# Performance work log

Hardware: AMD Instinct MI355X
Metric: run time of the kernel (lower is better)

## Reference

```python
import jax, jax.numpy as jnp
import numpy as np

B, L, D, H, V, NBARS = 128, 256, 256, 256, 130, 17


def _lstm(x, h, c, Wih, Whh, bih, bhh):
    # torch nn.LSTMCell math
    g = x @ Wih.T + h @ Whh.T + (bih + bhh)
    i, f, gg, o = jnp.split(g, 4, axis=-1)
    c2 = jax.nn.sigmoid(f) * c + jax.nn.sigmoid(i) * jnp.tanh(gg)
    return jax.nn.sigmoid(o) * jnp.tanh(c2), c2


def setup_inputs() -> dict:
    key = jax.random.key(0)
    ks = jax.random.split(key, 10)
    s = 0.05
    return dict(
        c=jax.random.normal(ks[0], (B, NBARS, D), jnp.float32),
        target=jax.random.randint(ks[1], (3, B, L), 0, V),
        length=L,
        W_hid=jax.random.normal(ks[2], (2 * D, D), jnp.float32) * s,
        b_hid=jnp.zeros((2 * D,), jnp.float32),
        W1_ih=jax.random.normal(ks[3], (3, 4 * H, 2 * D), jnp.float32) * s,
        W1_hh=jax.random.normal(ks[4], (3, 4 * H, H), jnp.float32) * s,
        b1_ih=jnp.zeros((3, 4 * H), jnp.float32),
        b1_hh=jnp.zeros((3, 4 * H), jnp.float32),
        Wc_ih=jax.random.normal(ks[5], (4 * H, 3 * H), jnp.float32) * s,
        Wc_hh=jax.random.normal(ks[6], (4 * H, H), jnp.float32) * s,
        bc_ih=jnp.zeros((4 * H,), jnp.float32),
        bc_hh=jnp.zeros((4 * H,), jnp.float32),
        emb=jax.random.normal(ks[7], (3, V, D), jnp.float32) * s,
        Wout=jax.random.normal(ks[8], (3, V, H), jnp.float32) * s,
        bout=jnp.zeros((3, V), jnp.float32),
    )


def _forward(c, W_hid, b_hid, W1_ih, W1_hh, b1_ih, b1_hh, Wc_ih, Wc_hh,
             bc_ih, bc_hh, emb, Wout, bout, target, length):
    Bsz = c.shape[0]
    # initial notes: embedding of token 0 for each of the 3 streams
    notes0 = jnp.broadcast_to(emb[:, 0, :][:, None, :], (3, Bsz, D))
    z3 = jnp.zeros((3, Bsz, H), c.dtype)
    z1 = jnp.zeros((Bsz, H), c.dtype)
    carry0 = (z3, z3, z3, z3, z1, z1, notes0)

    def step(carry, t):
        h1, c1, h2, c2, hc, cc, notes = carry
        bar = t // 16
        c_bar = jax.lax.dynamic_index_in_dim(c, bar, axis=1, keepdims=False)      # [B, D]
        c_t = jax.lax.dynamic_index_in_dim(c, bar + 1, axis=1, keepdims=False)    # [B, D]
        h_init = jnp.tanh(c_bar @ W_hid.T + b_hid)[:, :H]
        reset = (t % 16) == 0
        rs = lambda x: jnp.where(reset, jnp.broadcast_to(h_init, x.shape), x)
        zr = lambda x: jnp.where(reset, jnp.zeros_like(x), x)
        h1, c1, h2, c2, hc, cc = rs(h1), zr(c1), rs(h2), zr(c2), rs(hc), zr(cc)

        # first lstm1 update for all 3 streams (independent -> vmap)
        c_t3 = jnp.broadcast_to(c_t, (3,) + c_t.shape)
        x1 = jnp.concatenate([notes, c_t3], axis=-1)                               # [3, B, 2D]
        h1, c1 = jax.vmap(_lstm)(x1, h1, c1, W1_ih, W1_hh, b1_ih, b1_hh)

        tgt = jax.lax.dynamic_index_in_dim(target, t, axis=2, keepdims=False)      # [3, B]
        h1l = [h1[i] for i in range(3)]
        c1l = [c1[i] for i in range(3)]
        h2l = [h2[i] for i in range(3)]
        c2l = [c2[i] for i in range(3)]
        nl = [notes[i] for i in range(3)]
        outs = []
        # sequential dependency through the context cell -> small fixed loop of 3
        for i in range(3):
            hc, cc = _lstm(jnp.concatenate(h1l, axis=-1), hc, cc, Wc_ih, Wc_hh, bc_ih, bc_hh)
            h2l[i], c2l[i] = _lstm(jnp.concatenate([hc, c_t], axis=-1), h2l[i], c2l[i],
                                   W1_ih[i], W1_hh[i], b1_ih[i], b1_hh[i])
            outs.append((h1l[i] + h2l[i]) @ Wout[i].T + bout[i])                   # [B, V]
            nl[i] = emb[i][tgt[i]]                                                 # teacher forcing
            h1l[i], c1l[i] = _lstm(jnp.concatenate([nl[i], c_t], axis=-1), h1l[i], c1l[i],
                                   W1_ih[i], W1_hh[i], b1_ih[i], b1_hh[i])
        carry = (jnp.stack(h1l), jnp.stack(c1l), jnp.stack(h2l), jnp.stack(c2l),
                 hc, cc, jnp.stack(nl))
        return carry, jnp.stack(outs)                                              # [3, B, V]

    _, ys = jax.lax.scan(step, carry0, jnp.arange(length))                         # [L, 3, B, V]
    return jnp.transpose(ys, (1, 2, 0, 3))                                         # [3, B, L, V]


def reference(c, target, length, W_hid, b_hid, W1_ih, W1_hh, b1_ih, b1_hh,
              Wc_ih, Wc_hh, bc_ih, bc_hh, emb, Wout, bout):
    return _forward(c, W_hid, b_hid, W1_ih, W1_hh, b1_ih, b1_hh, Wc_ih, Wc_hh,
                    bc_ih, bc_hh, emb, Wout, bout, target, length)
```

## Files before the change

### kernel.cpp

```cpp
#include <hip/hip_runtime.h>
#include <hip/hip_bf16.h>

typedef float  f32x4  __attribute__((ext_vector_type(4)));
typedef short  short8 __attribute__((ext_vector_type(8)));
typedef short  bf4    __attribute__((ext_vector_type(4)));

#define MFMA16(a,b,c) __builtin_amdgcn_mfma_f32_16x16x32_bf16((a),(b),(c),0,0,0)

__device__ __forceinline__ short tobf(float f){
  unsigned u = __float_as_uint(f);
  u += 0x7fffu + ((u >> 16) & 1u);
  return (short)(u >> 16);
}
__device__ __forceinline__ float frombf(short s){
  return __uint_as_float(((unsigned)(unsigned short)s) << 16);
}
__device__ __forceinline__ float sigf(float x){
  return 1.f / (1.f + __expf(-x));
}
__device__ __forceinline__ float tanhf_(float x){
  float ax = fabsf(x);
  float e  = __expf(-2.f * ax);
  float t  = (1.f - e) / (1.f + e);
  return x >= 0.f ? t : -t;
}
__device__ __forceinline__ bf4 pack4(f32x4 v){
  bf4 r; r[0]=tobf(v[0]); r[1]=tobf(v[1]); r[2]=tobf(v[2]); r[3]=tobf(v[3]); return r;
}

__device__ __forceinline__ int hoff(int row, int col){
  return (row*512 + col*2) ^ ((row & 7) << 4);
}
__device__ __forceinline__ void stH(short* buf, int row, int col, short v){
  *(short*)((char*)buf + hoff(row,col)) = v;
}
__device__ __forceinline__ short8 ldA(const short* buf, int k0, int lane){
  int row = lane & 15;
  int off = (row*512 + (k0 + ((lane>>4)<<3))*2) ^ ((row & 7) << 4);
  return *(const short8*)((const char*)buf + off);
}
__device__ __forceinline__ short* cpPtr(short* cp, int s, int w, int g, int lane){
  return cp + (((s*16 + w)*4 + g) << 8) + (lane << 2);
}
__device__ __forceinline__ f32x4 ldCP(const short* cp, int s, int w, int g, int lane){
  bf4 v = *(const bf4*)(cp + (((s*16 + w)*4 + g) << 8) + (lane << 2));
  f32x4 r; r[0]=frombf(v[0]); r[1]=frombf(v[1]); r[2]=frombf(v[2]); r[3]=frombf(v[3]);
  return r;
}
__device__ __forceinline__ f32x4 ldCS(const float* b, int sl, int tid){
  return *(const f32x4*)(b + sl*4096 + tid*4);
}
__device__ __forceinline__ void stCS(float* b, int sl, int tid, f32x4 v){
  *(f32x4*)(b + sl*4096 + tid*4) = v;
}

__device__ __forceinline__ void gemm256(f32x4 (&acc)[4], const short* __restrict__ W,
                                        int KT, int kt0, const short* __restrict__ A,
                                        int lane, int w){
  const short* w0 = W + (((     w)*KT + kt0)*64 + lane)*8;
  const short* w1 = W + (((16 + w)*KT + kt0)*64 + lane)*8;
  const short* w2 = W + (((32 + w)*KT + kt0)*64 + lane)*8;
  const short* w3 = W + (((48 + w)*KT + kt0)*64 + lane)*8;
  short8 b0[4], b1[4], b2[4], b3[4];
#define GLD(B,K) do{ (B)[0]=*(const short8*)(w0+(K)*512); (B)[1]=*(const short8*)(w1+(K)*512); \
                     (B)[2]=*(const short8*)(w2+(K)*512); (B)[3]=*(const short8*)(w3+(K)*512);}while(0)
#define GMM(B,K) do{ short8 a0_=ldA(A,(K)*32,lane); \
  acc[0]=MFMA16(a0_,(B)[0],acc[0]); acc[1]=MFMA16(a0_,(B)[1],acc[1]); \
  acc[2]=MFMA16(a0_,(B)[2],acc[2]); acc[3]=MFMA16(a0_,(B)[3],acc[3]);}while(0)
  GLD(b0,0); GLD(b1,1); GLD(b2,2); GLD(b3,3);
  GMM(b0,0); GLD(b0,4);
  GMM(b1,1); GLD(b1,5);
  GMM(b2,2); GLD(b2,6);
  GMM(b3,3); GLD(b3,7);
  GMM(b0,4);
  GMM(b1,5);
  GMM(b2,6);
  GMM(b3,7);
#undef GLD
#undef GMM
}

__global__ void swz_kernel(short* __restrict__ dst, const float* __restrict__ src,
                           int rowStride, int colOff, int Nreal,
                           int KTtot, int kt0, int ktN, int NT){
  int idx = blockIdx.x*256 + threadIdx.x;
  if (idx >= NT*ktN*512) return;
  int j = idx & 7, l = (idx>>3) & 63, tile = idx >> 9;
  int nt = tile / ktN, ktl = tile - nt*ktN;
  int n = nt*16 + (l & 15);
  int k = ktl*32 + ((l>>4)<<3) + j;
  float v = (n < Nreal) ? src[n*rowStride + colOff + k] : 0.f;
  dst[(((nt*KTtot + kt0 + ktl)*64 + l)<<3) + j] = tobf(v);
}

__global__ __launch_bounds__(1024) void eproj_kernel(
    const float* __restrict__ emb, const float* __restrict__ b1_ih,
    const float* __restrict__ b1_hh, const short* __restrict__ W1ihA_s,
    short* __restrict__ eprojb){
  __shared__ short es[36864];
  const int s = blockIdx.x;
  const int tid = threadIdx.x, lane = tid & 63, w = tid >> 6;
  const int l15 = lane & 15, lg = lane >> 4;
  for (int idx = tid; idx < 36864; idx += 1024){
    int row = idx >> 8, c2 = idx & 255;
    float v = (row < 130) ? emb[(s*130 + row)*256 + c2] : 0.f;
    *(short*)((char*)es + ((row*512 + c2*2) ^ ((row & 7) << 4))) = tobf(v);
  }
  __syncthreads();
  f32x4 z4 = {0.f,0.f,0.f,0.f};
  for (int rt = 0; rt < 9; ++rt){
    const short* Arow = es + rt*4096;
    f32x4 acc[4] = {z4, z4, z4, z4};
    #pragma unroll 2
    for (int kt = 0; kt < 8; ++kt){
      short8 a = ldA(Arow, kt*32, lane);
      #pragma unroll
      for (int q = 0; q < 4; ++q){
        short8 b = *(const short8*)(W1ihA_s + s*262144 + (((w*4+q)*8 + kt)*64 + lane)*8);
        acc[q] = MFMA16(a, b, acc[q]);
      }
    }
    #pragma unroll
    for (int q = 0; q < 4; ++q)
      #pragma unroll
      for (int r = 0; r < 4; ++r){
        int v = rt*16 + lg*4 + r;
        if (v < 130){
          int gc = (w*4 + q)*16 + l15;
          eprojb[(s*130 + v)*1024 + ((gc & 255) << 2) + (gc >> 8)] =
            tobf(acc[q][r] + b1_ih[s*1024 + gc] + b1_hh[s*1024 + gc]);
        }
      }
  }
}

__global__ __launch_bounds__(1024)
__attribute__((amdgpu_waves_per_eu(4,4))) void rnn_main(
    const float* __restrict__ cbuf, const int* __restrict__ tgt,
    const float* __restrict__ b_hid, const float* __restrict__ b1_ih,
    const float* __restrict__ b1_hh, const float* __restrict__ bc_ih,
    const float* __restrict__ bc_hh, const float* __restrict__ boutp,
    const short* __restrict__ eprojb, short* __restrict__ cpart,
    float* __restrict__ cst,
    const short* __restrict__ W1hh_s, const short* __restrict__ W1ihA_s,
    const short* __restrict__ W1ihB_s, const short* __restrict__ Wc_s,
    const short* __restrict__ Whid_s, const short* __restrict__ Wout_s,
    float* __restrict__ outp)
{
  __shared__ short h1b[3*4096];
  __shared__ short h2b[3*4096];
  __shared__ short hcb[4096];

  const int tid  = threadIdx.x;
  const int lane = tid & 63;
  const int w    = tid >> 6;
  const int l15  = lane & 15;
  const int lg   = lane >> 4;
  const int chunk = blockIdx.x;
  const int bar   = blockIdx.y;
  const int b0    = chunk * 16;
  const int cc    = w*16 + l15;
  const int wgid  = bar*8 + chunk;

  short* cpWG  = cpart + wgid*49152;
  float* cstWG = cst + (size_t)wgid*28672;
  const f32x4 z4 = {0.f,0.f,0.f,0.f};

  #pragma unroll 1
  for (int tt = 0; tt < 16; ++tt){
    const int t = bar*16 + tt;

    if (tt == 0){
      for (int idx = tid; idx < 4096; idx += 1024){
        int row = idx >> 8, c2 = idx & 255;
        stH(h2b,        row, c2, tobf(cbuf[((b0+row)*17 + bar)*256 + c2]));
        stH(h2b + 4096, row, c2, tobf(cbuf[((b0+row)*17 + bar + 1)*256 + c2]));
      }
      __syncthreads();
      f32x4 hi0 = z4;
      #pragma unroll
      for (int kt = 0; kt < 8; ++kt){
        short8 a0 = ldA(h2b, kt*32, lane);
        short8 bb = *(const short8*)(Whid_s + ((w*8 + kt)*64 + lane)*8);
        hi0 = MFMA16(a0, bb, hi0);
      }
      #pragma unroll 1
      for (int s = 0; s < 3; ++s){
        f32x4 acc[4] = {z4, z4, z4, z4};
        gemm256(acc, W1ihB_s + s*262144, 8, 0, h2b + 4096, lane, w);
        #pragma unroll
        for (int g = 0; g < 4; ++g)
          *(bf4*)cpPtr(cpWG, s, w, g, lane) = pack4(acc[g]);
      }
      __syncthreads();
      {
        float bh = b_hid[cc];
        #pragma unroll
        for (int r = 0; r < 4; ++r){
          int row = lg*4 + r;
          short hv = tobf(tanhf_(hi0[r] + bh));
          stH(h1b,       row,cc,hv); stH(h1b+4096, row,cc,hv); stH(h1b+8192,row,cc,hv);
          stH(h2b,       row,cc,hv); stH(h2b+4096, row,cc,hv); stH(h2b+8192,row,cc,hv);
          stH(hcb,       row,cc,hv);
        }
      }
      __syncthreads();
    }

    #pragma unroll 1
    for (int s = 0; s < 3; ++s){
      f32x4 cold = tt ? ldCS(cstWG, s, tid) : z4;
      f32x4 acc[4];
      #pragma unroll
      for (int g = 0; g < 4; ++g) acc[g] = ldCP(cpWG, s, w, g, lane);
      gemm256(acc, W1hh_s + s*262144, 8, 0, h1b + s*4096, lane, w);
      __syncthreads();
      f32x4 cnew;
      #pragma unroll
      for (int r = 0; r < 4; ++r){
        const int row = lg*4 + r;
        const int tok = (t == 0) ? 0 : tgt[(s*128 + b0 + row)*256 + (t-1)];
        bf4 e4 = *(const bf4*)(eprojb + (size_t)(s*130 + tok)*1024 + cc*4);
        float pi = acc[0][r] + frombf(e4[0]);
        float pf = acc[1][r] + frombf(e4[1]);
        float pg = acc[2][r] + frombf(e4[2]);
        float po = acc[3][r] + frombf(e4[3]);
        float cs = sigf(pf)*cold[r] + sigf(pi)*tanhf_(pg);
        cnew[r] = cs;
        stH(h1b + s*4096, row, cc, tobf(sigf(po)*tanhf_(cs)));
      }
      stCS(cstWG, s, tid, cnew);
    }
    __syncthreads();

    #pragma unroll 1
    for (int i = 0; i < 3; ++i){
      {
        f32x4 cold = (tt == 0 && i == 0) ? z4 : ldCS(cstWG, 6, tid);
        f32x4 acc[4] = {z4, z4, z4, z4};
        #pragma unroll 1
        for (int seg = 0; seg < 4; ++seg){
          const short* Ax = (seg==0) ? h1b : (seg==1) ? (h1b+4096)
                           : (seg==2) ? (h1b+8192) : hcb;
          gemm256(acc, Wc_s, 32, seg*8, Ax, lane, w);
        }
        __syncthreads();
        const float bi = bc_ih[cc]      + bc_hh[cc];
        const float bf = bc_ih[256+cc]  + bc_hh[256+cc];
        const float bg = bc_ih[512+cc]  + bc_hh[512+cc];
        const float bo = bc_ih[768+cc]  + bc_hh[768+cc];
        f32x4 cnew;
        #pragma unroll
        for (int r = 0; r < 4; ++r){
          const int row = lg*4 + r;
          float cs = sigf(acc[1][r] + bf)*cold[r]
                   + sigf(acc[0][r] + bi)*tanhf_(acc[2][r] + bg);
          cnew[r] = cs;
          stH(hcb, row, cc, tobf(sigf(acc[3][r] + bo)*tanhf_(cs)));
        }
        stCS(cstWG, 6, tid, cnew);
        __syncthreads();
      }
      {
        f32x4 cold = (tt == 0) ? z4 : ldCS(cstWG, 3+i, tid);
        f32x4 acc[4];
        #pragma unroll
        for (int g = 0; g < 4; ++g) acc[g] = ldCP(cpWG, i, w, g, lane);
        gemm256(acc, W1ihA_s + i*262144, 8, 0, hcb, lane, w);
        gemm256(acc, W1hh_s  + i*262144, 8, 0, h2b + i*4096, lane, w);
        __syncthreads();
        const float bi = b1_ih[i*1024+cc]      + b1_hh[i*1024+cc];
        const float bf = b1_ih[i*1024+256+cc]  + b1_hh[i*1024+256+cc];
        const float bg = b1_ih[i*1024+512+cc]  + b1_hh[i*1024+512+cc];
        const float bo = b1_ih[i*1024+768+cc]  + b1_hh[i*1024+768+cc];
        f32x4 cnew;
        #pragma unroll
        for (int r = 0; r < 4; ++r){
          const int row = lg*4 + r;
          float cs = sigf(acc[1][r] + bf)*cold[r]
                   + sigf(acc[0][r] + bi)*tanhf_(acc[2][r] + bg);
          cnew[r] = cs;
          stH(h2b + i*4096, row, cc, tobf(sigf(acc[3][r] + bo)*tanhf_(cs)));
        }
        stCS(cstWG, 3+i, tid, cnew);
        __syncthreads();
      }
      {
        f32x4 cold = ldCS(cstWG, i, tid);
        f32x4 acc[4];
        #pragma unroll
        for (int g = 0; g < 4; ++g) acc[g] = ldCP(cpWG, i, w, g, lane);
        f32x4 e0 = z4;
        const short* WH = W1hh_s + i*262144;
        const short* wh0 = WH + (((     w)*8)*64 + lane)*8;
        const short* wh1 = WH + (((16+w)*8)*64 + lane)*8;
        const short* wh2 = WH + (((32+w)*8)*64 + lane)*8;
        const short* wh3 = WH + (((48+w)*8)*64 + lane)*8;
        const short* wo  = Wout_s + i*36864 + ((w*8)*64 + lane)*8;
        const short* h1p = h1b + i*4096;
        const short* h2p = h2b + i*4096;
        short8 hb0[4], hb1[4], hb2[4], hb3[4], ebA, ebB;
#define DLD(B,K) do{ (B)[0]=*(const short8*)(wh0+(K)*512); (B)[1]=*(const short8*)(wh1+(K)*512); \
                     (B)[2]=*(const short8*)(wh2+(K)*512); (B)[3]=*(const short8*)(wh3+(K)*512);}while(0)
#define DMM(B,EB,K) do{ \
  short8 a0_=ldA(h1p,(K)*32,lane); \
  acc[0]=MFMA16(a0_,(B)[0],acc[0]); acc[1]=MFMA16(a0_,(B)[1],acc[1]); \
  acc[2]=MFMA16(a0_,(B)[2],acc[2]); acc[3]=MFMA16(a0_,(B)[3],acc[3]); \
  if (w < 9){ short8 f0_=ldA(h2p,(K)*32,lane); \
    e0=MFMA16(a0_,(EB),e0); e0=MFMA16(f0_,(EB),e0); }}while(0)
        DLD(hb0,0); DLD(hb1,1); DLD(hb2,2); DLD(hb3,3);
        if (w < 9){ ebA = *(const short8*)(wo); ebB = *(const short8*)(wo+512); }
        DMM(hb0,ebA,0); DLD(hb0,4); if (w<9) ebA = *(const short8*)(wo+2*512);
        DMM(hb1,ebB,1); DLD(hb1,5); if (w<9) ebB = *(const short8*)(wo+3*512);
        DMM(hb2,ebA,2); DLD(hb2,6); if (w<9) ebA = *(const short8*)(wo+4*512);
        DMM(hb3,ebB,3); DLD(hb3,7); if (w<9) ebB = *(const short8*)(wo+5*512);
        DMM(hb0,ebA,4); if (w<9) ebA = *(const short8*)(wo+6*512);
        DMM(hb1,ebB,5); if (w<9) ebB = *(const short8*)(wo+7*512);
        DMM(hb2,ebA,6);
        DMM(hb3,ebB,7);
#undef DLD
#undef DMM
        __syncthreads();
        f32x4 cnew;
        #pragma unroll
        for (int r = 0; r < 4; ++r){
          const int row = lg*4 + r;
          const int tok = tgt[(i*128 + b0 + row)*256 + t];
          bf4 e4 = *(const bf4*)(eprojb + (size_t)(i*130 + tok)*1024 + cc*4);
          float pi = acc[0][r] + frombf(e4[0]);
          float pf = acc[1][r] + frombf(e4[1]);
          float pg = acc[2][r] + frombf(e4[2]);
          float po = acc[3][r] + frombf(e4[3]);
          float cs = sigf(pf)*cold[r] + sigf(pi)*tanhf_(pg);
          cnew[r] = cs;
          stH(h1b + i*4096, row, cc, tobf(sigf(po)*tanhf_(cs)));
        }
        stCS(cstWG, i, tid, cnew);
        if (w < 8){
          const int v = w*16 + l15;
          const float bo = boutp[i*130 + v];
          #pragma unroll
          for (int r = 0; r < 4; ++r){
            const int row = lg*4 + r;
            outp[(size_t)((i*128 + b0 + row)*256 + t)*130 + v] = e0[r] + bo;
          }
        } else if (w == 8 && l15 < 2){
          const int v = 128 + l15;
          const float bo = boutp[i*130 + v];
          #pragma unroll
          for (int r = 0; r < 4; ++r){
            const int row = lg*4 + r;
            outp[(size_t)((i*128 + b0 + row)*256 + t)*130 + v] = e0[r] + bo;
          }
        }
        __syncthreads();
      }
    }
  }
}

extern "C" void kernel_launch(void* const* d_in, const int* in_sizes, int n_in,
                              void* d_out, int out_size, void* d_ws, size_t ws_size,
                              hipStream_t stream){
  (void)in_sizes; (void)n_in; (void)out_size; (void)ws_size;
  const float* c     = (const float*)d_in[0];
  const int*   tgt   = (const int*)  d_in[1];
  const float* W_hid = (const float*)d_in[3];
  const float* b_hid = (const float*)d_in[4];
  const float* W1_ih = (const float*)d_in[5];
  const float* W1_hh = (const float*)d_in[6];
  const float* b1_ih = (const float*)d_in[7];
  const float* b1_hh = (const float*)d_in[8];
  const float* Wc_ih = (const float*)d_in[9];
  const float* Wc_hh = (const float*)d_in[10];
  const float* bc_ih = (const float*)d_in[11];
  const float* bc_hh = (const float*)d_in[12];
  const float* emb   = (const float*)d_in[13];
  const float* Wout  = (const float*)d_in[14];
  const float* bout  = (const float*)d_in[15];
  float* outp = (float*)d_out;

  short* ws = (short*)d_ws;
  short* W1hh_s  = ws;
  short* W1ihA_s = ws + 786432;
  short* W1ihB_s = ws + 1572864;
  short* Wc_s    = ws + 2359296;
  short* Whid_s  = ws + 3407872;
  short* Wout_s  = ws + 3473408;
  short* eprojb  = ws + 3584000;
  short* cpart   = ws + 3983360;
  float* cstate  = (float*)((char*)d_ws + 20549632);

  for (int s = 0; s < 3; ++s){
    swz_kernel<<<1024,256,0,stream>>>(W1hh_s  + s*262144, W1_hh + s*262144, 256,   0, 1024,  8, 0,  8, 64);
    swz_kernel<<<1024,256,0,stream>>>(W1ihA_s + s*262144, W1_ih + s*524288, 512,   0, 1024,  8, 0,  8, 64);
    swz_kernel<<<1024,256,0,stream>>>(W1ihB_s + s*262144, W1_ih + s*524288, 512, 256, 1024,  8, 0,  8, 64);
    swz_kernel<<< 144,256,0,stream>>>(Wout_s  + s*36864,  Wout  + s*33280,  256,   0,  130,  8, 0,  8,  9);
  }
  swz_kernel<<<3072,256,0,stream>>>(Wc_s,   Wc_ih, 768, 0, 1024, 32,  0, 24, 64);
  swz_kernel<<<1024,256,0,stream>>>(Wc_s,   Wc_hh, 256, 0, 1024, 32, 24,  8, 64);
  swz_kernel<<< 256,256,0,stream>>>(Whid_s, W_hid, 256, 0,  512,  8,  0,  8, 16);
  eproj_kernel<<<3,1024,0,stream>>>(emb, b1_ih, b1_hh, W1ihA_s, eprojb);

  rnn_main<<<dim3(8,16),1024,0,stream>>>(c, tgt, b_hid, b1_ih, b1_hh, bc_ih, bc_hh,
                                         bout, eprojb, cpart, cstate,
                                         W1hh_s, W1ihA_s, W1ihB_s,
                                         Wc_s, Whid_s, Wout_s, outp);
}
```

Measured before the change: 3.094 ms.

## Keep LSTM cell states in LDS and fully unroll weight-prefetched GEMM loops

Moves the h1 and conductor cell states (4 slices × 4096 floats) from the global scratch buffer into a new 64 KB shared-memory array, while the h2 cell states stay in global. The aim is to cut global read/write traffic on the per-step recurrence. It also replaces the four looped gemm256 calls for the conductor LSTM, and the two back-to-back gemm256 calls for the layer-2 LSTM, with single fully unrolled loops. These loops keep a rolling 4-deep prefetch of weights across segment boundaries, so pipeline bubbles between segments go away. The cost is much higher LDS use and more registers, which could hurt occupancy or fail under launch bounds of 1024 with waves_per_eu 4.

Result: slower. 7.089 ms (+129.1%).

```diff
diff --git a/kernel.cpp b/kernel.cpp
--- a/kernel.cpp
+++ b/kernel.cpp
@@ -51,6 +51,12 @@
   return *(const f32x4*)(b + sl*4096 + tid*4);
 }
 __device__ __forceinline__ void stCS(float* b, int sl, int tid, f32x4 v){
+  *(f32x4*)(b + sl*4096 + tid*4) = v;
+}
+__device__ __forceinline__ f32x4 ldCSL(const float* b, int sl, int tid){
+  return *(const f32x4*)(b + sl*4096 + tid*4);
+}
+__device__ __forceinline__ void stCSL(float* b, int sl, int tid, f32x4 v){
   *(f32x4*)(b + sl*4096 + tid*4) = v;
 }
 
@@ -150,6 +156,7 @@
   __shared__ short h1b[3*4096];
   __shared__ short h2b[3*4096];
   __shared__ short hcb[4096];
+  __shared__ float csb[4*4096];
 
   const int tid  = threadIdx.x;
   const int lane = tid & 63;
@@ -209,7 +216,7 @@
 
     #pragma unroll 1
     for (int s = 0; s < 3; ++s){
-      f32x4 cold = tt ? ldCS(cstWG, s, tid) : z4;
+      f32x4 cold = tt ? ldCSL(csb, s, tid) : z4;
       f32x4 acc[4];
       #pragma unroll
       for (int g = 0; g < 4; ++g) acc[g] = ldCP(cpWG, s, w, g, lane);
@@ -229,21 +236,35 @@
         cnew[r] = cs;
         stH(h1b + s*4096, row, cc, tobf(sigf(po)*tanhf_(cs)));
       }
-      stCS(cstWG, s, tid, cnew);
+      stCSL(csb, s, tid, cnew);
     }
     __syncthreads();
 
     #pragma unroll 1
     for (int i = 0; i < 3; ++i){
       {
-        f32x4 cold = (tt == 0 && i == 0) ? z4 : ldCS(cstWG, 6, tid);
+        f32x4 cold = (tt == 0 && i == 0) ? z4 : ldCSL(csb, 3, tid);
         f32x4 acc[4] = {z4, z4, z4, z4};
-        #pragma unroll 1
-        for (int seg = 0; seg < 4; ++seg){
-          const short* Ax = (seg==0) ? h1b : (seg==1) ? (h1b+4096)
-                           : (seg==2) ? (h1b+8192) : hcb;
-          gemm256(acc, Wc_s, 32, seg*8, Ax, lane, w);
-        }
+        const short* w0 = Wc_s + (((     w)*32)*64 + lane)*8;
+        const short* w1 = Wc_s + (((16 + w)*32)*64 + lane)*8;
+        const short* w2 = Wc_s + (((32 + w)*32)*64 + lane)*8;
+        const short* w3 = Wc_s + (((48 + w)*32)*64 + lane)*8;
+        short8 b0[4], b1[4], b2[4], b3[4];
+#define BROT(K) (((K)&3)==0?b0:(((K)&3)==1?b1:(((K)&3)==2?b2:b3)))
+#define GLDW(B,K) do{ (B)[0]=*(const short8*)(w0+(K)*512); (B)[1]=*(const short8*)(w1+(K)*512); \
+                      (B)[2]=*(const short8*)(w2+(K)*512); (B)[3]=*(const short8*)(w3+(K)*512);}while(0)
+#define GMMW(B,A,K) do{ short8 a0_=ldA((A),(K)*32,lane); \
+  acc[0]=MFMA16(a0_,(B)[0],acc[0]); acc[1]=MFMA16(a0_,(B)[1],acc[1]); \
+  acc[2]=MFMA16(a0_,(B)[2],acc[2]); acc[3]=MFMA16(a0_,(B)[3],acc[3]);}while(0)
+        GLDW(b0,0); GLDW(b1,1); GLDW(b2,2); GLDW(b3,3);
+        #pragma unroll
+        for (int k = 0; k < 32; ++k){
+          const short* Ax = (k<8) ? h1b : (k<16) ? (h1b+4096) : (k<24) ? (h1b+8192) : hcb;
+          GMMW(BROT(k), Ax, k & 7);
+          if (k < 28) GLDW(BROT(k+4), k+4);
+        }
+#undef GLDW
+#undef GMMW
         __syncthreads();
         const float bi = bc_ih[cc]      + bc_hh[cc];
         const float bf = bc_ih[256+cc]  + bc_hh[256+cc];
@@ -258,16 +279,44 @@
           cnew[r] = cs;
           stH(hcb, row, cc, tobf(sigf(acc[3][r] + bo)*tanhf_(cs)));
         }
-        stCS(cstWG, 6, tid, cnew);
+        stCSL(csb, 3, tid, cnew);
         __syncthreads();
       }
       {
-        f32x4 cold = (tt == 0) ? z4 : ldCS(cstWG, 3+i, tid);
+        f32x4 cold = (tt == 0) ? z4 : ldCS(cstWG, i, tid);
         f32x4 acc[4];
         #pragma unroll
         for (int g = 0; g < 4; ++g) acc[g] = ldCP(cpWG, i, w, g, lane);
-        gemm256(acc, W1ihA_s + i*262144, 8, 0, hcb, lane, w);
-        gemm256(acc, W1hh_s  + i*262144, 8, 0, h2b + i*4096, lane, w);
+        const short* WA = W1ihA_s + i*262144;
+        const short* WH = W1hh_s  + i*262144;
+        const short* wa0 = WA + (((     w)*8)*64 + lane)*8;
+        const short* wa1 = WA + (((16+w)*8)*64 + lane)*8;
+        const short* wa2 = WA + (((32+w)*8)*64 + lane)*8;
+        const short* wa3 = WA + (((48+w)*8)*64 + lane)*8;
+        const short* wh0 = WH + (((     w)*8)*64 + lane)*8;
+        const short* wh1 = WH + (((16+w)*8)*64 + lane)*8;
+        const short* wh2 = WH + (((32+w)*8)*64 + lane)*8;
+        const short* wh3 = WH + (((48+w)*8)*64 + lane)*8;
+        short8 b0[4], b1[4], b2[4], b3[4];
+        const short* h2p = h2b + i*4096;
+#define GLDC(B,K) do{ if ((K) < 8){ \
+    (B)[0]=*(const short8*)(wa0+(K)*512); (B)[1]=*(const short8*)(wa1+(K)*512); \
+    (B)[2]=*(const short8*)(wa2+(K)*512); (B)[3]=*(const short8*)(wa3+(K)*512); \
+  } else { \
+    (B)[0]=*(const short8*)(wh0+((K)-8)*512); (B)[1]=*(const short8*)(wh1+((K)-8)*512); \
+    (B)[2]=*(const short8*)(wh2+((K)-8)*512); (B)[3]=*(const short8*)(wh3+((K)-8)*512); }}while(0)
+#define GMMC(B,K) do{ const short* Ax_ = ((K)<8) ? hcb : h2p; \
+  short8 a0_=ldA(Ax_,((K)&7)*32,lane); \
+  acc[0]=MFMA16(a0_,(B)[0],acc[0]); acc[1]=MFMA16(a0_,(B)[1],acc[1]); \
+  acc[2]=MFMA16(a0_,(B)[2],acc[2]); acc[3]=MFMA16(a0_,(B)[3],acc[3]);}while(0)
+        GLDC(b0,0); GLDC(b1,1); GLDC(b2,2); GLDC(b3,3);
+        #pragma unroll
+        for (int k = 0; k < 16; ++k){
+          GMMC(BROT(k), k);
+          if (k < 12) GLDC(BROT(k+4), k+4);
+        }
+#undef GLDC
+#undef GMMC
         __syncthreads();
         const float bi = b1_ih[i*1024+cc]      + b1_hh[i*1024+cc];
         const float bf = b1_ih[i*1024+256+cc]  + b1_hh[i*1024+256+cc];
@@ -282,11 +331,11 @@
           cnew[r] = cs;
           stH(h2b + i*4096, row, cc, tobf(sigf(acc[3][r] + bo)*tanhf_(cs)));
         }
-        stCS(cstWG, 3+i, tid, cnew);
+        stCS(cstWG, i, tid, cnew);
         __syncthreads();
       }
       {
-        f32x4 cold = ldCS(cstWG, i, tid);
+        f32x4 cold = ldCSL(csb, i, tid);
         f32x4 acc[4];
         #pragma unroll
         for (int g = 0; g < 4; ++g) acc[g] = ldCP(cpWG, i, w, g, lane);
@@ -335,7 +384,7 @@
           cnew[r] = cs;
           stH(h1b + i*4096, row, cc, tobf(sigf(po)*tanhf_(cs)));
         }
-        stCS(cstWG, i, tid, cnew);
+        stCSL(csb, i, tid, cnew);
         if (w < 8){
           const int v = w*16 + l15;
           const float bo = boutp[i*130 + v];
@@ -357,6 +406,7 @@
       }
     }
   }
+#undef BROT
 }
 
 extern "C" void kernel_launch(void* const* d_in, const int* in_sizes, int n_in,
```

## Reuse partial conductor sums across substeps and fuse dual W1_hh GEMMs

Applied to the files above, without the earlier changes.

The conductor LSTM GEMM over the three h1 segments is now computed incrementally. Partial sums for segments that do not change between substeps are cached in registers as bf16 and reused, so fewer K-tiles are recomputed per substep. The h2 and h1 recurrent GEMMs that share W1_hh are merged into one dual-accumulator loop, so each weight fragment is loaded from global memory once instead of twice. This relies on h1 segments staying unchanged during the intermediate substeps. Storing the cached partials as bf16 adds rounding error and raises register pressure.

After: 4.327 ms. 39.8% more time.

```diff
diff --git a/kernel.cpp b/kernel.cpp
--- a/kernel.cpp
+++ b/kernel.cpp
@@ -27,6 +27,10 @@
 __device__ __forceinline__ bf4 pack4(f32x4 v){
   bf4 r; r[0]=tobf(v[0]); r[1]=tobf(v[1]); r[2]=tobf(v[2]); r[3]=tobf(v[3]); return r;
 }
+__device__ __forceinline__ f32x4 unpack4(bf4 v){
+  f32x4 r; r[0]=frombf(v[0]); r[1]=frombf(v[1]); r[2]=frombf(v[2]); r[3]=frombf(v[3]);
+  return r;
+}
 
 __device__ __forceinline__ int hoff(int row, int col){
   return (row*512 + col*2) ^ ((row & 7) << 4);
@@ -43,9 +47,7 @@
   return cp + (((s*16 + w)*4 + g) << 8) + (lane << 2);
 }
 __device__ __forceinline__ f32x4 ldCP(const short* cp, int s, int w, int g, int lane){
-  bf4 v = *(const bf4*)(cp + (((s*16 + w)*4 + g) << 8) + (lane << 2));
-  f32x4 r; r[0]=frombf(v[0]); r[1]=frombf(v[1]); r[2]=frombf(v[2]); r[3]=frombf(v[3]);
-  return r;
+  return unpack4(*(const bf4*)(cp + (((s*16 + w)*4 + g) << 8) + (lane << 2)));
 }
 __device__ __forceinline__ f32x4 ldCS(const float* b, int sl, int tid){
   return *(const f32x4*)(b + sl*4096 + tid*4);
@@ -78,6 +80,36 @@
   GMM(b3,7);
 #undef GLD
 #undef GMM
+}
+
+__device__ __forceinline__ void gemm256_dual(f32x4 (&acc)[4], f32x4 (&dacc)[4],
+                                             const short* __restrict__ W,
+                                             const short* __restrict__ A1,
+                                             const short* __restrict__ A2,
+                                             int lane, int w){
+  const short* w0 = W + ((     w)*8*64 + lane)*8;
+  const short* w1 = W + ((16 + w)*8*64 + lane)*8;
+  const short* w2 = W + ((32 + w)*8*64 + lane)*8;
+  const short* w3 = W + ((48 + w)*8*64 + lane)*8;
+  short8 b0[4], b1[4];
+#define DLD2(B,K) do{ (B)[0]=*(const short8*)(w0+(K)*512); (B)[1]=*(const short8*)(w1+(K)*512); \
+                      (B)[2]=*(const short8*)(w2+(K)*512); (B)[3]=*(const short8*)(w3+(K)*512);}while(0)
+#define DMM2(B,K) do{ short8 a1_=ldA(A1,(K)*32,lane); short8 a2_=ldA(A2,(K)*32,lane); \
+  acc[0]=MFMA16(a1_,(B)[0],acc[0]);  dacc[0]=MFMA16(a2_,(B)[0],dacc[0]); \
+  acc[1]=MFMA16(a1_,(B)[1],acc[1]);  dacc[1]=MFMA16(a2_,(B)[1],dacc[1]); \
+  acc[2]=MFMA16(a1_,(B)[2],acc[2]);  dacc[2]=MFMA16(a2_,(B)[2],dacc[2]); \
+  acc[3]=MFMA16(a1_,(B)[3],acc[3]);  dacc[3]=MFMA16(a2_,(B)[3],dacc[3]);}while(0)
+  DLD2(b0,0); DLD2(b1,1);
+  DMM2(b0,0); DLD2(b0,2);
+  DMM2(b1,1); DLD2(b1,3);
+  DMM2(b0,2); DLD2(b0,4);
+  DMM2(b1,3); DLD2(b1,5);
+  DMM2(b0,4); DLD2(b0,6);
+  DMM2(b1,5); DLD2(b1,7);
+  DMM2(b0,6);
+  DMM2(b1,7);
+#undef DLD2
+#undef DMM2
 }
 
 __global__ void swz_kernel(short* __restrict__ dst, const float* __restrict__ src,
@@ -233,17 +265,34 @@
     }
     __syncthreads();
 
+    bf4 p2b[4], p12b[4];
+
     #pragma unroll 1
     for (int i = 0; i < 3; ++i){
       {
         f32x4 cold = (tt == 0 && i == 0) ? z4 : ldCS(cstWG, 6, tid);
-        f32x4 acc[4] = {z4, z4, z4, z4};
-        #pragma unroll 1
-        for (int seg = 0; seg < 4; ++seg){
-          const short* Ax = (seg==0) ? h1b : (seg==1) ? (h1b+4096)
-                           : (seg==2) ? (h1b+8192) : hcb;
-          gemm256(acc, Wc_s, 32, seg*8, Ax, lane, w);
-        }
+        f32x4 acc[4];
+        if (i == 0){
+          #pragma unroll
+          for (int g = 0; g < 4; ++g) acc[g] = z4;
+          gemm256(acc, Wc_s, 32, 16, h1b + 8192, lane, w);
+          #pragma unroll
+          for (int g = 0; g < 4; ++g) p2b[g] = pack4(acc[g]);
+          gemm256(acc, Wc_s, 32, 8,  h1b + 4096, lane, w);
+          #pragma unroll
+          for (int g = 0; g < 4; ++g) p12b[g] = pack4(acc[g]);
+          gemm256(acc, Wc_s, 32, 0,  h1b,        lane, w);
+        } else if (i == 1){
+          #pragma unroll
+          for (int g = 0; g < 4; ++g) acc[g] = unpack4(p12b[g]);
+          gemm256(acc, Wc_s, 32, 0,  h1b,        lane, w);
+        } else {
+          #pragma unroll
+          for (int g = 0; g < 4; ++g) acc[g] = unpack4(p2b[g]);
+          gemm256(acc, Wc_s, 32, 0,  h1b,        lane, w);
+          gemm256(acc, Wc_s, 32, 8,  h1b + 4096, lane, w);
+        }
+        gemm256(acc, Wc_s, 32, 24, hcb, lane, w);
         __syncthreads();
         const float bi = bc_ih[cc]      + bc_hh[cc];
         const float bf = bc_ih[256+cc]  + bc_hh[256+cc];
@@ -261,13 +310,14 @@
         stCS(cstWG, 6, tid, cnew);
         __syncthreads();
       }
+      f32x4 dacc[4];
       {
         f32x4 cold = (tt == 0) ? z4 : ldCS(cstWG, 3+i, tid);
         f32x4 acc[4];
         #pragma unroll
-        for (int g = 0; g < 4; ++g) acc[g] = ldCP(cpWG, i, w, g, lane);
+        for (int g = 0; g < 4; ++g){ acc[g] = ldCP(cpWG, i, w, g, lane); dacc[g] = acc[g]; }
         gemm256(acc, W1ihA_s + i*262144, 8, 0, hcb, lane, w);
-        gemm256(acc, W1hh_s  + i*262144, 8, 0, h2b + i*4096, lane, w);
+        gemm256_dual(acc, dacc, W1hh_s + i*262144, h2b + i*4096, h1b + i*4096, lane, w);
         __syncthreads();
         const float bi = b1_ih[i*1024+cc]      + b1_hh[i*1024+cc];
         const float bf = b1_ih[i*1024+256+cc]  + b1_hh[i*1024+256+cc];
@@ -287,39 +337,25 @@
       }
       {
         f32x4 cold = ldCS(cstWG, i, tid);
-        f32x4 acc[4];
-        #pragma unroll
-        for (int g = 0; g < 4; ++g) acc[g] = ldCP(cpWG, i, w, g, lane);
         f32x4 e0 = z4;
-        const short* WH = W1hh_s + i*262144;
-        const short* wh0 = WH + (((     w)*8)*64 + lane)*8;
-        const short* wh1 = WH + (((16+w)*8)*64 + lane)*8;
-        const short* wh2 = WH + (((32+w)*8)*64 + lane)*8;
-        const short* wh3 = WH + (((48+w)*8)*64 + lane)*8;
-        const short* wo  = Wout_s + i*36864 + ((w*8)*64 + lane)*8;
         const short* h1p = h1b + i*4096;
         const short* h2p = h2b + i*4096;
-        short8 hb0[4], hb1[4], hb2[4], hb3[4], ebA, ebB;
-#define DLD(B,K) do{ (B)[0]=*(const short8*)(wh0+(K)*512); (B)[1]=*(const short8*)(wh1+(K)*512); \
-                     (B)[2]=*(const short8*)(wh2+(K)*512); (B)[3]=*(const short8*)(wh3+(K)*512);}while(0)
-#define DMM(B,EB,K) do{ \
-  short8 a0_=ldA(h1p,(K)*32,lane); \
-  acc[0]=MFMA16(a0_,(B)[0],acc[0]); acc[1]=MFMA16(a0_,(B)[1],acc[1]); \
-  acc[2]=MFMA16(a0_,(B)[2],acc[2]); acc[3]=MFMA16(a0_,(B)[3],acc[3]); \
-  if (w < 9){ short8 f0_=ldA(h2p,(K)*32,lane); \
-    e0=MFMA16(a0_,(EB),e0); e0=MFMA16(f0_,(EB),e0); }}while(0)
-        DLD(hb0,0); DLD(hb1,1); DLD(hb2,2); DLD(hb3,3);
-        if (w < 9){ ebA = *(const short8*)(wo); ebB = *(const short8*)(wo+512); }
-        DMM(hb0,ebA,0); DLD(hb0,4); if (w<9) ebA = *(const short8*)(wo+2*512);
-        DMM(hb1,ebB,1); DLD(hb1,5); if (w<9) ebB = *(const short8*)(wo+3*512);
-        DMM(hb2,ebA,2); DLD(hb2,6); if (w<9) ebA = *(const short8*)(wo+4*512);
-        DMM(hb3,ebB,3); DLD(hb3,7); if (w<9) ebB = *(const short8*)(wo+5*512);
-        DMM(hb0,ebA,4); if (w<9) ebA = *(const short8*)(wo+6*512);
-        DMM(hb1,ebB,5); if (w<9) ebB = *(const short8*)(wo+7*512);
-        DMM(hb2,ebA,6);
-        DMM(hb3,ebB,7);
-#undef DLD
-#undef DMM
+        if (w < 9){
+          const short* wo = Wout_s + i*36864 + ((w*8)*64 + lane)*8;
+          short8 ebA = *(const short8*)(wo);
+          short8 ebB = *(const short8*)(wo + 512);
+#define EMM(EB,K) do{ short8 a_=ldA(h1p,(K)*32,lane), f_=ldA(h2p,(K)*32,lane); \
+  e0 = MFMA16(a_,(EB),e0); e0 = MFMA16(f_,(EB),e0); }while(0)
+          EMM(ebA,0); ebA = *(const short8*)(wo + 2*512);
+          EMM(ebB,1); ebB = *(const short8*)(wo + 3*512);
+          EMM(ebA,2); ebA = *(const short8*)(wo + 4*512);
+          EMM(ebB,3); ebB = *(const short8*)(wo + 5*512);
+          EMM(ebA,4); ebA = *(const short8*)(wo + 6*512);
+          EMM(ebB,5); ebB = *(const short8*)(wo + 7*512);
+          EMM(ebA,6);
+          EMM(ebB,7);
+#undef EMM
+        }
         __syncthreads();
         f32x4 cnew;
         #pragma unroll
@@ -327,10 +363,10 @@
           const int row = lg*4 + r;
           const int tok = tgt[(i*128 + b0 + row)*256 + t];
           bf4 e4 = *(const bf4*)(eprojb + (size_t)(i*130 + tok)*1024 + cc*4);
-          float pi = acc[0][r] + frombf(e4[0]);
-          float pf = acc[1][r] + frombf(e4[1]);
-          float pg = acc[2][r] + frombf(e4[2]);
-          float po = acc[3][r] + frombf(e4[3]);
+          float pi = dacc[0][r] + frombf(e4[0]);
+          float pf = dacc[1][r] + frombf(e4[1]);
+          float pg = dacc[2][r] + frombf(e4[2]);
+          float po = dacc[3][r] + frombf(e4[3]);
           float cs = sigf(pf)*cold[r] + sigf(pi)*tanhf_(pg);
           cnew[r] = cs;
           stH(h1b + i*4096, row, cc, tobf(sigf(po)*tanhf_(cs)));
```
